# Kernel optimization log

Measured on AMD Instinct MI355X. Metric: run time of the kernel, lower is better.

## Reference

```python
import jax, jax.numpy as jnp
import numpy as np

NEG_SLOPE = 0.2


def _segment_softmax(logits, seg, num_segments):
    m = jax.ops.segment_max(logits, seg, num_segments=num_segments)
    m = jnp.where(jnp.isfinite(m), m, 0.0)
    e = jnp.exp(logits - m[seg])
    s = jax.ops.segment_sum(e, seg, num_segments=num_segments)
    return e / (s[seg] + 1e-16)


def _gat_conv(x, src, dst, W, a_src, a_dst, b, num_nodes):
    # PyG GATConv, heads=1, concat=True, add_self_loops already applied to src/dst.
    h = x @ W                                  # [N, F_out]
    alpha_src = h @ a_src                      # [N]
    alpha_dst = h @ a_dst                      # [N]
    logits = jax.nn.leaky_relu(alpha_src[src] + alpha_dst[dst], NEG_SLOPE)  # [E]
    alpha = _segment_softmax(logits, dst, num_nodes)                        # [E]
    out = jax.ops.segment_sum(alpha[:, None] * h[src], dst, num_segments=num_nodes)
    return out + b


def setup_inputs() -> dict:
    key = jax.random.key(0)
    ks = jax.random.split(key, 16)
    N, E, F_in = 50000, 1600000, 256
    x = jax.random.normal(ks[0], (N, F_in), dtype=jnp.float32)
    edge_index = jax.random.randint(ks[1], (2, E), 0, N, dtype=jnp.int64)
    edge_attr = jax.random.normal(ks[2], (E, 1), dtype=jnp.float32)

    def glorot(k, shape):
        fan = sum(shape) if len(shape) > 1 else shape[0]
        return jax.random.normal(k, shape, dtype=jnp.float32) * jnp.sqrt(2.0 / fan)

    params = {
        "W1": glorot(ks[3], (F_in, 48)), "as1": glorot(ks[4], (48,)),
        "ad1": glorot(ks[5], (48,)),     "b1": jnp.zeros((48,), jnp.float32),
        "W2": glorot(ks[6], (48, 60)),   "as2": glorot(ks[7], (60,)),
        "ad2": glorot(ks[8], (60,)),     "b2": jnp.zeros((60,), jnp.float32),
        "W3": glorot(ks[9], (60, 1)),    "as3": glorot(ks[10], (1,)),
        "ad3": glorot(ks[11], (1,)),     "b3": jnp.zeros((1,), jnp.float32),
    }
    return {"x": x, "edge_index": edge_index, "edge_attr": edge_attr, **params}


def reference(x, edge_index, edge_attr, W1, as1, ad1, b1, W2, as2, ad2, b2, W3, as3, ad3, b3):
    # edge_attr is accepted but ignored: GATConv was built without edge_dim, so no lin_edge.
    N = x.shape[0]
    loops = jnp.arange(N, dtype=edge_index.dtype)
    src = jnp.concatenate([edge_index[0], loops])  # add_self_loops=True
    dst = jnp.concatenate([edge_index[1], loops])
    h = jax.nn.relu(_gat_conv(x, src, dst, W1, as1, ad1, b1, N))
    h = jax.nn.relu(_gat_conv(h, src, dst, W2, as2, ad2, b2, N))
    h = _gat_conv(h, src, dst, W3, as3, ad3, b3, N)
    return h.reshape(-1)  # flatten -> [N]
```

## Files before the change

kernel.cpp:

```cpp
#include <hip/hip_runtime.h>
#include <cstdint>
#include <cstddef>


__device__ __forceinline__ float leaky(float v) { return v > 0.f ? v : 0.2f * v; }

__device__ __forceinline__ unsigned short f2bf(float x) {
    unsigned int u = __float_as_uint(x);
    u = (u + 0x7FFFu + ((u >> 16) & 1u)) >> 16;
    return (unsigned short)u;
}
__device__ __forceinline__ float bf2f(unsigned short b) {
    return __uint_as_float(((unsigned int)b) << 16);
}
__device__ __forceinline__ float bfhi(unsigned int d) {
    return __uint_as_float(d & 0xFFFF0000u);
}
__device__ __forceinline__ float bflo(unsigned int d) {
    return __uint_as_float(d << 16);
}

typedef _Float16 half8 __attribute__((ext_vector_type(8)));
typedef float f32x4 __attribute__((ext_vector_type(4)));

#define BSHIFT 7
#define BCAP   5120
#define CTILE  8192


__global__ __launch_bounds__(256) void coarse_bin_kernel(
    const int* __restrict__ ei, unsigned int* __restrict__ staged,
    int* __restrict__ gcursor, int E, int K) {
    __shared__ int hist[512];
    __shared__ int rank[512];
    __shared__ int base[512];
    for (int b = threadIdx.x; b < K; b += 256) { hist[b] = 0; rank[b] = 0; }
    __syncthreads();

    int e0 = blockIdx.x * CTILE;
    int e1 = min(E, e0 + CTILE);

    for (int e = e0 + threadIdx.x; e < e1; e += 256) {
        int d = ei[E + e];
        atomicAdd(&hist[d >> BSHIFT], 1);
    }
    __syncthreads();

    for (int b = threadIdx.x; b < K; b += 256) {
        int c = hist[b];
        base[b] = c ? atomicAdd(&gcursor[b], c) : 0;
    }
    __syncthreads();

    for (int e = e0 + threadIdx.x; e < e1; e += 256) {
        int s = ei[e];
        int d = ei[E + e];
        int b = d >> BSHIFT;
        int r = atomicAdd(&rank[b], 1);
        staged[(size_t)b * BCAP + base[b] + r] =
            ((unsigned int)(d & ((1 << BSHIFT) - 1)) << 16) | (unsigned int)s;
    }
}


__global__ __launch_bounds__(512) void bucket_scan_kernel(
    const int* __restrict__ gcursor, int* __restrict__ bbase, int K) {
    __shared__ int sh[512];
    int t = threadIdx.x;
    int v = (t < K) ? gcursor[t] : 0;
    sh[t] = v;
    __syncthreads();
    for (int off = 1; off < 512; off <<= 1) {
        int a = (t >= off) ? sh[t - off] : 0;
        __syncthreads();
        sh[t] += a;
        __syncthreads();
    }
    if (t < K) bbase[t] = sh[t] - v;
}


__global__ __launch_bounds__(256) void fine_sort_kernel(
    const unsigned int* __restrict__ staged, const int* __restrict__ gcursor,
    const int* __restrict__ bbase, int* __restrict__ rowptr, int* __restrict__ csr,
    int N, int E) {
    __shared__ int cnt[128];
    __shared__ int off[128];
    __shared__ int lcsr[BCAP];
    const int b = blockIdx.x;
    const int t = threadIdx.x;
    const int c = gcursor[b];
    const int gb = bbase[b];
    const unsigned int* rec = staged + (size_t)b * BCAP;

    if (t < 128) cnt[t] = 0;
    __syncthreads();

    for (int i = t; i < c; i += 256) atomicAdd(&cnt[rec[i] >> 16], 1);
    __syncthreads();

    if (t < 128) off[t] = cnt[t];
    __syncthreads();
    for (int s = 1; s < 128; s <<= 1) {
        int a = (t >= s && t < 128) ? off[t - s] : 0;
        __syncthreads();
        if (t < 128) off[t] += a;
        __syncthreads();
    }

    if (t < 128) {
        int excl = off[t] - cnt[t];
        int n = (b << BSHIFT) + t;
        if (n <= N) rowptr[n] = gb + excl;
        cnt[t] = excl;
    }
    if (b == 0 && t == 0) rowptr[N] = E;
    __syncthreads();

    for (int i = t; i < c; i += 256) {
        unsigned int r = rec[i];
        int p = atomicAdd(&cnt[r >> 16], 1);
        lcsr[p] = (int)(r & 0xFFFFu);
    }
    __syncthreads();

    for (int i = t; i < c; i += 256) csr[gb + i] = lcsr[i];
}


template <int FIN>
__global__ __launch_bounds__(256) void gemm1_mfma_kernel(
    const float* __restrict__ X, const float* __restrict__ W,
    const float* __restrict__ avs, const float* __restrict__ avd,
    unsigned short* __restrict__ hb, float* __restrict__ asrc, float* __restrict__ adst,
    int N) {
    constexpr int FOUT = 48;
    constexpr int KK = FIN / 32;
    static_assert(FIN % 32 == 0, "FIN multiple of 32");

    const int wid  = __builtin_amdgcn_readfirstlane(threadIdx.x >> 6);
    const int lane = threadIdx.x & 63;
    const int col  = lane & 15;
    const int grp  = lane >> 4;
    const int wbase = blockIdx.x * 64 + wid * 16;

    int arow = wbase + col;
    if (arow >= N) arow = N - 1;
    const float* xrow = X + (size_t)arow * FIN + grp * 8;

    half8 Bf[3][KK];
#pragma unroll
    for (int t = 0; t < 3; t++) {
#pragma unroll
        for (int kk = 0; kk < KK; kk++) {
            const float* wp = W + (size_t)(kk * 32 + grp * 8) * FOUT + t * 16 + col;
#pragma unroll
            for (int j = 0; j < 8; j++)
                Bf[t][kk][j] = (_Float16)wp[(size_t)j * FOUT];
        }
    }

    f32x4 acc0 = {0.f, 0.f, 0.f, 0.f};
    f32x4 acc1 = {0.f, 0.f, 0.f, 0.f};
    f32x4 acc2 = {0.f, 0.f, 0.f, 0.f};

#pragma unroll
    for (int kk = 0; kk < KK; kk++) {
        float4 xa = *(const float4*)(xrow + kk * 32);
        float4 xb = *(const float4*)(xrow + kk * 32 + 4);
        float xs[8] = {xa.x, xa.y, xa.z, xa.w, xb.x, xb.y, xb.z, xb.w};
        half8 ah, al;
#pragma unroll
        for (int j = 0; j < 8; j++) {
            _Float16 h = (_Float16)xs[j];
            ah[j] = h;
            al[j] = (_Float16)(xs[j] - (float)h);
        }
        acc0 = __builtin_amdgcn_mfma_f32_16x16x32_f16(ah, Bf[0][kk], acc0, 0, 0, 0);
        acc1 = __builtin_amdgcn_mfma_f32_16x16x32_f16(ah, Bf[1][kk], acc1, 0, 0, 0);
        acc2 = __builtin_amdgcn_mfma_f32_16x16x32_f16(ah, Bf[2][kk], acc2, 0, 0, 0);
        acc0 = __builtin_amdgcn_mfma_f32_16x16x32_f16(al, Bf[0][kk], acc0, 0, 0, 0);
        acc1 = __builtin_amdgcn_mfma_f32_16x16x32_f16(al, Bf[1][kk], acc1, 0, 0, 0);
        acc2 = __builtin_amdgcn_mfma_f32_16x16x32_f16(al, Bf[2][kk], acc2, 0, 0, 0);
    }

    float avs0 = avs[col], avs1 = avs[16 + col], avs2 = avs[32 + col];
    float avd0 = avd[col], avd1 = avd[16 + col], avd2 = avd[32 + col];

#pragma unroll
    for (int r = 0; r < 4; r++) {
        float ps = acc0[r] * avs0 + acc1[r] * avs1 + acc2[r] * avs2;
        float pd = acc0[r] * avd0 + acc1[r] * avd1 + acc2[r] * avd2;
#pragma unroll
        for (int off = 8; off; off >>= 1) {
            ps += __shfl_xor(ps, off, 64);
            pd += __shfl_xor(pd, off, 64);
        }
        int nd = wbase + grp * 4 + r;
        if (col == r && nd < N) { asrc[nd] = ps; adst[nd] = pd; }
    }

#pragma unroll
    for (int r = 0; r < 4; r++) {
        int nd = wbase + grp * 4 + r;
        if (nd < N) {
            unsigned short* hp = hb + (size_t)nd * 64 + col;
            hp[0]  = f2bf(acc0[r]);
            hp[16] = f2bf(acc1[r]);
            hp[32] = f2bf(acc2[r]);
        }
    }
}


template <int FIN, int FOUT, int FT>
__global__ __launch_bounds__(256) void gemm_sgpr_kernel(
    const float* __restrict__ X, const float* __restrict__ W,
    const float* __restrict__ avs, const float* __restrict__ avd,
    unsigned short* __restrict__ hb, float* __restrict__ asrc, float* __restrict__ adst,
    int N) {
    static_assert(4 * FT == FOUT, "FT must be FOUT/4");
    __shared__ float red[2][4][64];

    const int wid  = __builtin_amdgcn_readfirstlane(threadIdx.x >> 6);
    const int lane = threadIdx.x & 63;
    const int n    = blockIdx.x * 64 + lane;
    const int nc   = (n < N) ? n : N - 1;
    const int fbase = wid * FT;

    const float* xrow = X + (size_t)nc * FIN;

    float acc[FT];
#pragma unroll
    for (int c = 0; c < FT; c++) acc[c] = 0.f;

#pragma unroll
    for (int k = 0; k < FIN; k += 4) {
        float4 xv = *(const float4*)(xrow + k);
        const float* w0 = W + (size_t)k * FOUT + fbase;
#pragma unroll
        for (int c = 0; c < FT; c++) {
            acc[c] = fmaf(xv.x, w0[c],            acc[c]);
            acc[c] = fmaf(xv.y, w0[FOUT + c],     acc[c]);
            acc[c] = fmaf(xv.z, w0[2 * FOUT + c], acc[c]);
            acc[c] = fmaf(xv.w, w0[3 * FOUT + c], acc[c]);
        }
    }

    float ps = 0.f, pd = 0.f;
#pragma unroll
    for (int c = 0; c < FT; c++) {
        ps = fmaf(acc[c], avs[fbase + c], ps);
        pd = fmaf(acc[c], avd[fbase + c], pd);
    }
    red[0][wid][lane] = ps;
    red[1][wid][lane] = pd;

    if (n < N) {
        if constexpr ((FT & 1) == 0) {
            unsigned int* dst = (unsigned int*)(hb + (size_t)n * 64 + fbase);
#pragma unroll
            for (int c = 0; c < FT; c += 2) {
                unsigned int pk = (unsigned int)f2bf(acc[c]) |
                                  ((unsigned int)f2bf(acc[c + 1]) << 16);
                dst[c >> 1] = pk;
            }
        } else {
#pragma unroll
            for (int c = 0; c < FT; c++)
                hb[(size_t)n * 64 + fbase + c] = f2bf(acc[c]);
        }
    }

    __syncthreads();
    if (threadIdx.x < 64 && n < N) {
        float s = red[0][0][lane] + red[0][1][lane] + red[0][2][lane] + red[0][3][lane];
        float d = red[1][0][lane] + red[1][1][lane] + red[1][2][lane] + red[1][3][lane];
        asrc[n] = s;
        adst[n] = d;
    }
}


#define GATHER_STEP(NG)                                                        \
    {                                                                          \
        int   off_[NG];                                                        \
        uint2 hd_[NG];                                                         \
        float ww_[NG];                                                         \
        _Pragma("unroll")                                                      \
        for (int u = 0; u < NG; u++) off_[u] = offlds[wv][4 * u + q];          \
        _Pragma("unroll")                                                      \
        for (int u = 0; u < NG; u++)                                           \
            hd_[u] = *(const uint2*)(hbb + ((unsigned int)off_[u] + suboff));  \
        float we = (lane < cnt) ? __expf(leaky(as + ad_n)) : 0.f;              \
        wpart += we;                                                           \
        wlds[wv][lane] = we;                                                   \
        _Pragma("unroll")                                                      \
        for (int u = 0; u < NG; u++) ww_[u] = wlds[wv][4 * u + q];             \
        _Pragma("unroll")                                                      \
        for (int u = 0; u < NG; u++) {                                         \
            a0 = fmaf(ww_[u], bflo(hd_[u].x), a0);                             \
            a1 = fmaf(ww_[u], bfhi(hd_[u].x), a1);                             \
            a2 = fmaf(ww_[u], bflo(hd_[u].y), a2);                             \
            a3 = fmaf(ww_[u], bfhi(hd_[u].y), a3);                             \
        }                                                                      \
    }

template <int FOUT, bool RELU>
__global__ __launch_bounds__(256) void agg_pipe_kernel(
    const int* __restrict__ rowptr, const int* __restrict__ csr,
    const float* __restrict__ asrc, const float* __restrict__ adst,
    const unsigned short* __restrict__ hb, const float* __restrict__ bias,
    float* __restrict__ OUT, int N) {
    constexpr int NSUB = FOUT / 4;
    static_assert(FOUT % 4 == 0, "FOUT multiple of 4");
    __shared__ int   offlds[4][64];
    __shared__ float wlds[4][64];
    const int wv = threadIdx.x >> 6;
    int n = blockIdx.x * 4 + wv;
    if (n >= N) return;
    const int lane = threadIdx.x & 63;
    const int q    = lane >> 4;
    const int sub  = lane & 15;
    const int subc = (sub < NSUB) ? sub : NSUB - 1;
    const unsigned int suboff = (unsigned int)subc * 8;
    const int rs = rowptr[n], re = rowptr[n + 1];
    const float ad_n = adst[n];
    const float wself = __expf(leaky(asrc[n] + ad_n));
    const char* hbb = (const char*)hb;

    float a0 = 0.f, a1 = 0.f, a2 = 0.f, a3 = 0.f;
    float wpart = 0.f;

    for (int base = rs; base < re; base += 64) {
        const int cnt = min(64, re - base);
        int ce = base + lane;
        if (ce >= re) ce = re - 1;
        int sv = csr[ce];
        int sidx = (lane < cnt) ? sv : n;
        offlds[wv][lane] = sidx << 7;
        float as = asrc[sidx];
        if (cnt <= 32) { GATHER_STEP(8) } else { GATHER_STEP(16) }
    }

#pragma unroll
    for (int off = 32; off; off >>= 1) wpart += __shfl_xor(wpart, off, 64);
    const float ssum = wpart + wself;

    a0 += __shfl_xor(a0, 16, 64); a0 += __shfl_xor(a0, 32, 64);
    a1 += __shfl_xor(a1, 16, 64); a1 += __shfl_xor(a1, 32, 64);
    a2 += __shfl_xor(a2, 16, 64); a2 += __shfl_xor(a2, 32, 64);
    a3 += __shfl_xor(a3, 16, 64); a3 += __shfl_xor(a3, 32, 64);

    {
        uint2 sv = *(const uint2*)(hbb + (((unsigned int)n << 7) + suboff));
        a0 = fmaf(wself, bflo(sv.x), a0);
        a1 = fmaf(wself, bfhi(sv.x), a1);
        a2 = fmaf(wself, bflo(sv.y), a2);
        a3 = fmaf(wself, bfhi(sv.y), a3);
    }

    if (lane < NSUB) {
        const float inv = 1.f / (ssum + 1e-16f);
        float4 bv = *(const float4*)(bias + sub * 4);
        float4 o;
        o.x = a0 * inv + bv.x;
        o.y = a1 * inv + bv.y;
        o.z = a2 * inv + bv.z;
        o.w = a3 * inv + bv.w;
        if (RELU) {
            o.x = fmaxf(o.x, 0.f); o.y = fmaxf(o.y, 0.f);
            o.z = fmaxf(o.z, 0.f); o.w = fmaxf(o.w, 0.f);
        }
        *(float4*)(OUT + (size_t)n * FOUT + sub * 4) = o;
    }
}


__global__ __launch_bounds__(256) void agg_pipe_h3_kernel(
    const int* __restrict__ rowptr, const int* __restrict__ csr,
    const float* __restrict__ asrc, const float* __restrict__ adst,
    const unsigned short* __restrict__ hb, const float* __restrict__ bias,
    const float* __restrict__ W3, float* __restrict__ h3, int N) {
    constexpr int FOUT = 60;
    constexpr int NSUB = FOUT / 4;
    __shared__ int   offlds[4][64];
    __shared__ float wlds[4][64];
    const int wv = threadIdx.x >> 6;
    int n = blockIdx.x * 4 + wv;
    if (n >= N) return;
    const int lane = threadIdx.x & 63;
    const int q    = lane >> 4;
    const int sub  = lane & 15;
    const int subc = (sub < NSUB) ? sub : NSUB - 1;
    const unsigned int suboff = (unsigned int)subc * 8;
    const int rs = rowptr[n], re = rowptr[n + 1];
    const float ad_n = adst[n];
    const float wself = __expf(leaky(asrc[n] + ad_n));
    const char* hbb = (const char*)hb;

    float a0 = 0.f, a1 = 0.f, a2 = 0.f, a3 = 0.f;
    float wpart = 0.f;

    for (int base = rs; base < re; base += 64) {
        const int cnt = min(64, re - base);
        int ce = base + lane;
        if (ce >= re) ce = re - 1;
        int sv = csr[ce];
        int sidx = (lane < cnt) ? sv : n;
        offlds[wv][lane] = sidx << 7;
        float as = asrc[sidx];
        if (cnt <= 32) { GATHER_STEP(8) } else { GATHER_STEP(16) }
    }

#pragma unroll
    for (int off = 32; off; off >>= 1) wpart += __shfl_xor(wpart, off, 64);
    const float ssum = wpart + wself;

    a0 += __shfl_xor(a0, 16, 64); a0 += __shfl_xor(a0, 32, 64);
    a1 += __shfl_xor(a1, 16, 64); a1 += __shfl_xor(a1, 32, 64);
    a2 += __shfl_xor(a2, 16, 64); a2 += __shfl_xor(a2, 32, 64);
    a3 += __shfl_xor(a3, 16, 64); a3 += __shfl_xor(a3, 32, 64);

    {
        uint2 sv = *(const uint2*)(hbb + (((unsigned int)n << 7) + suboff));
        a0 = fmaf(wself, bflo(sv.x), a0);
        a1 = fmaf(wself, bfhi(sv.x), a1);
        a2 = fmaf(wself, bflo(sv.y), a2);
        a3 = fmaf(wself, bfhi(sv.y), a3);
    }

    float t = 0.f;
    {
        const float inv = 1.f / (ssum + 1e-16f);
        float4 bv = *(const float4*)(bias + subc * 4);
        float4 wv3 = *(const float4*)(W3 + subc * 4);
        float o0 = fmaxf(a0 * inv + bv.x, 0.f);
        float o1 = fmaxf(a1 * inv + bv.y, 0.f);
        float o2 = fmaxf(a2 * inv + bv.z, 0.f);
        float o3 = fmaxf(a3 * inv + bv.w, 0.f);
        if (sub < NSUB)
            t = o0 * wv3.x + o1 * wv3.y + o2 * wv3.z + o3 * wv3.w;
    }
#pragma unroll
    for (int off = 8; off; off >>= 1) t += __shfl_xor(t, off, 64);
    if (lane == 0) h3[n] = t;
}


__global__ __launch_bounds__(256) void agg1_kernel(
    const int* __restrict__ rowptr, const int* __restrict__ csr,
    const float* __restrict__ h3,
    const float* __restrict__ as3p, const float* __restrict__ ad3p,
    const float* __restrict__ bias, float* __restrict__ OUT, int N) {
    int n = blockIdx.x * 4 + (threadIdx.x >> 6);
    if (n >= N) return;
    int lane = threadIdx.x & 63;
    int rs = rowptr[n], re = rowptr[n + 1];
    const float a_s = as3p[0];
    float hn = h3[n];
    float adn = ad3p[0] * hn;
    float wself = __expf(leaky(a_s * hn + adn));

    float ssum = 0.f, accv = 0.f;
    for (int e = rs + lane; e < re; e += 64) {
        float hs = h3[csr[e]];
        float w = __expf(leaky(a_s * hs + adn));
        ssum += w;
        accv = fmaf(w, hs, accv);
    }
#pragma unroll
    for (int off = 32; off; off >>= 1) {
        ssum += __shfl_xor(ssum, off, 64);
        accv += __shfl_xor(accv, off, 64);
    }
    ssum += wself;
    accv = fmaf(wself, hn, accv);
    if (lane == 0) OUT[n] = accv / (ssum + 1e-16f) + bias[0];
}


extern "C" void kernel_launch(void* const* d_in, const int* in_sizes, int n_in,
                              void* d_out, int out_size, void* d_ws, size_t ws_size,
                              hipStream_t stream) {
    const float* x      = (const float*)d_in[0];
    const int*   ei     = (const int*)d_in[1];
    const float* W1  = (const float*)d_in[3];
    const float* as1 = (const float*)d_in[4];
    const float* ad1 = (const float*)d_in[5];
    const float* b1  = (const float*)d_in[6];
    const float* W2  = (const float*)d_in[7];
    const float* as2 = (const float*)d_in[8];
    const float* ad2 = (const float*)d_in[9];
    const float* b2  = (const float*)d_in[10];
    const float* W3  = (const float*)d_in[11];
    const float* as3 = (const float*)d_in[12];
    const float* ad3 = (const float*)d_in[13];
    const float* b3  = (const float*)d_in[14];

    const int N = in_sizes[0] / 256;
    const int E = in_sizes[1] / 2;
    const int K = (N + (1 << BSHIFT) - 1) >> BSHIFT;

    char* p = (char*)d_ws;
    auto alloc = [&](size_t bytes) -> void* {
        void* r = (void*)p;
        p += ((bytes + 255) / 256) * 256;
        return r;
    };
    int*   gcursor = (int*)alloc(512 * 4);
    int*   bbase   = (int*)alloc(512 * 4);
    int*   rowptr  = (int*)alloc(((size_t)N + 1) * 4);
    int*   csr     = (int*)alloc((size_t)E * 4);
    unsigned short* hb = (unsigned short*)alloc((size_t)N * 64 * 2);
    float* actbuf  = (float*)alloc((size_t)N * 48 * 4);
    float* h3      = (float*)alloc((size_t)N * 4);
    float* asrc    = (float*)alloc((size_t)N * 4);
    float* adst    = (float*)alloc((size_t)N * 4);
    unsigned int* staged = (unsigned int*)actbuf;

    hipMemsetAsync(gcursor, 0, 512 * 4, stream);
    int cblocks = (E + CTILE - 1) / CTILE;
    coarse_bin_kernel<<<cblocks, 256, 0, stream>>>(ei, staged, gcursor, E, K);
    bucket_scan_kernel<<<1, 512, 0, stream>>>(gcursor, bbase, K);
    fine_sort_kernel<<<K, 256, 0, stream>>>(staged, gcursor, bbase, rowptr, csr, N, E);

    int gblocks = (N + 63) / 64;
    int ablocks = (N + 3) / 4;

    gemm1_mfma_kernel<256><<<gblocks, 256, 0, stream>>>(
        x, W1, as1, ad1, hb, asrc, adst, N);
    agg_pipe_kernel<48, true><<<ablocks, 256, 0, stream>>>(rowptr, csr, asrc, adst, hb, b1, actbuf, N);

    gemm_sgpr_kernel<48, 60, 15><<<gblocks, 256, 0, stream>>>(
        actbuf, W2, as2, ad2, hb, asrc, adst, N);
    agg_pipe_h3_kernel<<<ablocks, 256, 0, stream>>>(rowptr, csr, asrc, adst, hb, b2, W3, h3, N);

    agg1_kernel<<<ablocks, 256, 0, stream>>>(rowptr, csr, h3, as3, ad3, b3, (float*)d_out, N);
}
```

Baseline: 267.6 us.

## Co-launch coarse binning with layer-1 GEMM and fold bucket scan into fine sort

The coarse edge-binning kernel and the first-layer MFMA GEMM are merged into one launch, with block-index ranges split between the two independent jobs so they can overlap on the GPU. The separate single-block bucket-scan kernel is removed; each fine-sort block now computes its global base by summing the preceding bucket counts itself. This cuts two kernel launches and their serialization gaps. In exchange, fine-sort blocks do redundant prefix sums over up to ~400 counts, and the fused kernel's register/LDS footprint is the union of both paths, which may reduce occupancy.

```diff
diff --git a/kernel.cpp b/kernel.cpp
--- a/kernel.cpp
+++ b/kernel.cpp
@@ -28,73 +28,149 @@
 #define CTILE  8192
 
 
-__global__ __launch_bounds__(256) void coarse_bin_kernel(
+template <int FIN>
+__global__ __launch_bounds__(256) void coarse_gemm1_kernel(
     const int* __restrict__ ei, unsigned int* __restrict__ staged,
-    int* __restrict__ gcursor, int E, int K) {
-    __shared__ int hist[512];
-    __shared__ int rank[512];
-    __shared__ int base[512];
-    for (int b = threadIdx.x; b < K; b += 256) { hist[b] = 0; rank[b] = 0; }
-    __syncthreads();
-
-    int e0 = blockIdx.x * CTILE;
-    int e1 = min(E, e0 + CTILE);
-
-    for (int e = e0 + threadIdx.x; e < e1; e += 256) {
-        int d = ei[E + e];
-        atomicAdd(&hist[d >> BSHIFT], 1);
-    }
-    __syncthreads();
-
-    for (int b = threadIdx.x; b < K; b += 256) {
-        int c = hist[b];
-        base[b] = c ? atomicAdd(&gcursor[b], c) : 0;
-    }
-    __syncthreads();
-
-    for (int e = e0 + threadIdx.x; e < e1; e += 256) {
-        int s = ei[e];
-        int d = ei[E + e];
-        int b = d >> BSHIFT;
-        int r = atomicAdd(&rank[b], 1);
-        staged[(size_t)b * BCAP + base[b] + r] =
-            ((unsigned int)(d & ((1 << BSHIFT) - 1)) << 16) | (unsigned int)s;
-    }
-}
-
-
-__global__ __launch_bounds__(512) void bucket_scan_kernel(
-    const int* __restrict__ gcursor, int* __restrict__ bbase, int K) {
-    __shared__ int sh[512];
-    int t = threadIdx.x;
-    int v = (t < K) ? gcursor[t] : 0;
-    sh[t] = v;
-    __syncthreads();
-    for (int off = 1; off < 512; off <<= 1) {
-        int a = (t >= off) ? sh[t - off] : 0;
+    int* __restrict__ gcursor, int E, int K, int cblocks,
+    const float* __restrict__ X, const float* __restrict__ W,
+    const float* __restrict__ avs, const float* __restrict__ avd,
+    unsigned short* __restrict__ hb, float* __restrict__ asrc,
+    float* __restrict__ adst, int N) {
+
+    if ((int)blockIdx.x < cblocks) {
+        __shared__ int hist[512];
+        __shared__ int rank[512];
+        __shared__ int base[512];
+        for (int b = threadIdx.x; b < K; b += 256) { hist[b] = 0; rank[b] = 0; }
         __syncthreads();
-        sh[t] += a;
+
+        int e0 = blockIdx.x * CTILE;
+        int e1 = min(E, e0 + CTILE);
+
+        for (int e = e0 + threadIdx.x; e < e1; e += 256) {
+            int d = ei[E + e];
+            atomicAdd(&hist[d >> BSHIFT], 1);
+        }
         __syncthreads();
-    }
-    if (t < K) bbase[t] = sh[t] - v;
+
+        for (int b = threadIdx.x; b < K; b += 256) {
+            int c = hist[b];
+            base[b] = c ? atomicAdd(&gcursor[b], c) : 0;
+        }
+        __syncthreads();
+
+        for (int e = e0 + threadIdx.x; e < e1; e += 256) {
+            int s = ei[e];
+            int d = ei[E + e];
+            int b = d >> BSHIFT;
+            int r = atomicAdd(&rank[b], 1);
+            staged[(size_t)b * BCAP + base[b] + r] =
+                ((unsigned int)(d & ((1 << BSHIFT) - 1)) << 16) | (unsigned int)s;
+        }
+        return;
+    }
+
+    constexpr int FOUT = 48;
+    constexpr int KK = FIN / 32;
+    static_assert(FIN % 32 == 0, "FIN multiple of 32");
+
+    const int bid  = (int)blockIdx.x - cblocks;
+    const int wid  = __builtin_amdgcn_readfirstlane(threadIdx.x >> 6);
+    const int lane = threadIdx.x & 63;
+    const int col  = lane & 15;
+    const int grp  = lane >> 4;
+    const int wbase = bid * 64 + wid * 16;
+
+    int arow = wbase + col;
+    if (arow >= N) arow = N - 1;
+    const float* xrow = X + (size_t)arow * FIN + grp * 8;
+
+    half8 Bf[3][KK];
+#pragma unroll
+    for (int t = 0; t < 3; t++) {
+#pragma unroll
+        for (int kk = 0; kk < KK; kk++) {
+            const float* wp = W + (size_t)(kk * 32 + grp * 8) * FOUT + t * 16 + col;
+#pragma unroll
+            for (int j = 0; j < 8; j++)
+                Bf[t][kk][j] = (_Float16)wp[(size_t)j * FOUT];
+        }
+    }
+
+    f32x4 acc0 = {0.f, 0.f, 0.f, 0.f};
+    f32x4 acc1 = {0.f, 0.f, 0.f, 0.f};
+    f32x4 acc2 = {0.f, 0.f, 0.f, 0.f};
+
+#pragma unroll
+    for (int kk = 0; kk < KK; kk++) {
+        float4 xa = *(const float4*)(xrow + kk * 32);
+        float4 xb = *(const float4*)(xrow + kk * 32 + 4);
+        float xs[8] = {xa.x, xa.y, xa.z, xa.w, xb.x, xb.y, xb.z, xb.w};
+        half8 ah, al;
+#pragma unroll
+        for (int j = 0; j < 8; j++) {
+            _Float16 h = (_Float16)xs[j];
+            ah[j] = h;
+            al[j] = (_Float16)(xs[j] - (float)h);
+        }
+        acc0 = __builtin_amdgcn_mfma_f32_16x16x32_f16(ah, Bf[0][kk], acc0, 0, 0, 0);
+        acc1 = __builtin_amdgcn_mfma_f32_16x16x32_f16(ah, Bf[1][kk], acc1, 0, 0, 0);
+        acc2 = __builtin_amdgcn_mfma_f32_16x16x32_f16(ah, Bf[2][kk], acc2, 0, 0, 0);
+        acc0 = __builtin_amdgcn_mfma_f32_16x16x32_f16(al, Bf[0][kk], acc0, 0, 0, 0);
+        acc1 = __builtin_amdgcn_mfma_f32_16x16x32_f16(al, Bf[1][kk], acc1, 0, 0, 0);
+        acc2 = __builtin_amdgcn_mfma_f32_16x16x32_f16(al, Bf[2][kk], acc2, 0, 0, 0);
+    }
+
+    float avs0 = avs[col], avs1 = avs[16 + col], avs2 = avs[32 + col];
+    float avd0 = avd[col], avd1 = avd[16 + col], avd2 = avd[32 + col];
+
+#pragma unroll
+    for (int r = 0; r < 4; r++) {
+        float ps = acc0[r] * avs0 + acc1[r] * avs1 + acc2[r] * avs2;
+        float pd = acc0[r] * avd0 + acc1[r] * avd1 + acc2[r] * avd2;
+#pragma unroll
+        for (int off = 8; off; off >>= 1) {
+            ps += __shfl_xor(ps, off, 64);
+            pd += __shfl_xor(pd, off, 64);
+        }
+        int nd = wbase + grp * 4 + r;
+        if (col == r && nd < N) { asrc[nd] = ps; adst[nd] = pd; }
+    }
+
+#pragma unroll
+    for (int r = 0; r < 4; r++) {
+        int nd = wbase + grp * 4 + r;
+        if (nd < N) {
+            unsigned short* hp = hb + (size_t)nd * 64 + col;
+            hp[0]  = f2bf(acc0[r]);
+            hp[16] = f2bf(acc1[r]);
+            hp[32] = f2bf(acc2[r]);
+        }
+    }
 }
 
 
 __global__ __launch_bounds__(256) void fine_sort_kernel(
     const unsigned int* __restrict__ staged, const int* __restrict__ gcursor,
-    const int* __restrict__ bbase, int* __restrict__ rowptr, int* __restrict__ csr,
-    int N, int E) {
+    int* __restrict__ rowptr, int* __restrict__ csr, int N, int E) {
     __shared__ int cnt[128];
     __shared__ int off[128];
+    __shared__ int gbred[4];
     __shared__ int lcsr[BCAP];
     const int b = blockIdx.x;
     const int t = threadIdx.x;
     const int c = gcursor[b];
-    const int gb = bbase[b];
     const unsigned int* rec = staged + (size_t)b * BCAP;
+
+    int pacc = 0;
+    for (int i = t; i < b; i += 256) pacc += gcursor[i];
+#pragma unroll
+    for (int o2 = 32; o2; o2 >>= 1) pacc += __shfl_xor(pacc, o2, 64);
+    if ((t & 63) == 0) gbred[t >> 6] = pacc;
 
     if (t < 128) cnt[t] = 0;
     __syncthreads();
+    const int gb = gbred[0] + gbred[1] + gbred[2] + gbred[3];
 
     for (int i = t; i < c; i += 256) atomicAdd(&cnt[rec[i] >> 16], 1);
     __syncthreads();
@@ -125,91 +201,6 @@
     __syncthreads();
 
     for (int i = t; i < c; i += 256) csr[gb + i] = lcsr[i];
-}
-
-
-template <int FIN>
-__global__ __launch_bounds__(256) void gemm1_mfma_kernel(
-    const float* __restrict__ X, const float* __restrict__ W,
-    const float* __restrict__ avs, const float* __restrict__ avd,
-    unsigned short* __restrict__ hb, float* __restrict__ asrc, float* __restrict__ adst,
-    int N) {
-    constexpr int FOUT = 48;
-    constexpr int KK = FIN / 32;
-    static_assert(FIN % 32 == 0, "FIN multiple of 32");
-
-    const int wid  = __builtin_amdgcn_readfirstlane(threadIdx.x >> 6);
-    const int lane = threadIdx.x & 63;
-    const int col  = lane & 15;
-    const int grp  = lane >> 4;
-    const int wbase = blockIdx.x * 64 + wid * 16;
-
-    int arow = wbase + col;
-    if (arow >= N) arow = N - 1;
-    const float* xrow = X + (size_t)arow * FIN + grp * 8;
-
-    half8 Bf[3][KK];
-#pragma unroll
-    for (int t = 0; t < 3; t++) {
-#pragma unroll
-        for (int kk = 0; kk < KK; kk++) {
-            const float* wp = W + (size_t)(kk * 32 + grp * 8) * FOUT + t * 16 + col;
-#pragma unroll
-            for (int j = 0; j < 8; j++)
-                Bf[t][kk][j] = (_Float16)wp[(size_t)j * FOUT];
-        }
-    }
-
-    f32x4 acc0 = {0.f, 0.f, 0.f, 0.f};
-    f32x4 acc1 = {0.f, 0.f, 0.f, 0.f};
-    f32x4 acc2 = {0.f, 0.f, 0.f, 0.f};
-
-#pragma unroll
-    for (int kk = 0; kk < KK; kk++) {
-        float4 xa = *(const float4*)(xrow + kk * 32);
-        float4 xb = *(const float4*)(xrow + kk * 32 + 4);
-        float xs[8] = {xa.x, xa.y, xa.z, xa.w, xb.x, xb.y, xb.z, xb.w};
-        half8 ah, al;
-#pragma unroll
-        for (int j = 0; j < 8; j++) {
-            _Float16 h = (_Float16)xs[j];
-            ah[j] = h;
-            al[j] = (_Float16)(xs[j] - (float)h);
-        }
-        acc0 = __builtin_amdgcn_mfma_f32_16x16x32_f16(ah, Bf[0][kk], acc0, 0, 0, 0);
-        acc1 = __builtin_amdgcn_mfma_f32_16x16x32_f16(ah, Bf[1][kk], acc1, 0, 0, 0);
-        acc2 = __builtin_amdgcn_mfma_f32_16x16x32_f16(ah, Bf[2][kk], acc2, 0, 0, 0);
-        acc0 = __builtin_amdgcn_mfma_f32_16x16x32_f16(al, Bf[0][kk], acc0, 0, 0, 0);
-        acc1 = __builtin_amdgcn_mfma_f32_16x16x32_f16(al, Bf[1][kk], acc1, 0, 0, 0);
-        acc2 = __builtin_amdgcn_mfma_f32_16x16x32_f16(al, Bf[2][kk], acc2, 0, 0, 0);
-    }
-
-    float avs0 = avs[col], avs1 = avs[16 + col], avs2 = avs[32 + col];
-    float avd0 = avd[col], avd1 = avd[16 + col], avd2 = avd[32 + col];
-
-#pragma unroll
-    for (int r = 0; r < 4; r++) {
-        float ps = acc0[r] * avs0 + acc1[r] * avs1 + acc2[r] * avs2;
-        float pd = acc0[r] * avd0 + acc1[r] * avd1 + acc2[r] * avd2;
-#pragma unroll
-        for (int off = 8; off; off >>= 1) {
-            ps += __shfl_xor(ps, off, 64);
-            pd += __shfl_xor(pd, off, 64);
-        }
-        int nd = wbase + grp * 4 + r;
-        if (col == r && nd < N) { asrc[nd] = ps; adst[nd] = pd; }
-    }
-
-#pragma unroll
-    for (int r = 0; r < 4; r++) {
-        int nd = wbase + grp * 4 + r;
-        if (nd < N) {
-            unsigned short* hp = hb + (size_t)nd * 64 + col;
-            hp[0]  = f2bf(acc0[r]);
-            hp[16] = f2bf(acc1[r]);
-            hp[32] = f2bf(acc2[r]);
-        }
-    }
 }
 
 
@@ -306,6 +297,7 @@
         }                                                                      \
     }
 
+
 template <int FOUT, bool RELU>
 __global__ __launch_bounds__(256) void agg_pipe_kernel(
     const int* __restrict__ rowptr, const int* __restrict__ csr,
@@ -509,7 +501,6 @@
         return r;
     };
     int*   gcursor = (int*)alloc(512 * 4);
-    int*   bbase   = (int*)alloc(512 * 4);
     int*   rowptr  = (int*)alloc(((size_t)N + 1) * 4);
     int*   csr     = (int*)alloc((size_t)E * 4);
     unsigned short* hb = (unsigned short*)alloc((size_t)N * 64 * 2);
@@ -521,20 +512,21 @@
 
     hipMemsetAsync(gcursor, 0, 512 * 4, stream);
     int cblocks = (E + CTILE - 1) / CTILE;
-    coarse_bin_kernel<<<cblocks, 256, 0, stream>>>(ei, staged, gcursor, E, K);
-    bucket_scan_kernel<<<1, 512, 0, stream>>>(gcursor, bbase, K);
-    fine_sort_kernel<<<K, 256, 0, stream>>>(staged, gcursor, bbase, rowptr, csr, N, E);
-
     int gblocks = (N + 63) / 64;
+    coarse_gemm1_kernel<256><<<cblocks + gblocks, 256, 0, stream>>>(
+        ei, staged, gcursor, E, K, cblocks,
+        x, W1, as1, ad1, hb, asrc, adst, N);
+    fine_sort_kernel<<<K, 256, 0, stream>>>(staged, gcursor, rowptr, csr, N, E);
+
     int ablocks = (N + 3) / 4;
 
-    gemm1_mfma_kernel<256><<<gblocks, 256, 0, stream>>>(
-        x, W1, as1, ad1, hb, asrc, adst, N);
-    agg_pipe_kernel<48, true><<<ablocks, 256, 0, stream>>>(rowptr, csr, asrc, adst, hb, b1, actbuf, N);
+    agg_pipe_kernel<48, true><<<ablocks, 256, 0, stream>>>(
+        rowptr, csr, asrc, adst, hb, b1, actbuf, N);
 
     gemm_sgpr_kernel<48, 60, 15><<<gblocks, 256, 0, stream>>>(
         actbuf, W2, as2, ad2, hb, asrc, adst, N);
-    agg_pipe_h3_kernel<<<ablocks, 256, 0, stream>>>(rowptr, csr, asrc, adst, hb, b2, W3, h3, N);
+    agg_pipe_h3_kernel<<<ablocks, 256, 0, stream>>>(
+        rowptr, csr, asrc, adst, hb, b2, W3, h3, N);
 
     agg1_kernel<<<ablocks, 256, 0, stream>>>(rowptr, csr, h3, as3, ad3, b3, (float*)d_out, N);
 }
```

Result: faster. 257.5 us (median of 2 runs) (-3.8%).
